# Performance work log

Measured on AMD Instinct MI355X. Metric: run time of the kernel, lower is better.

## Reference

```python
import jax, jax.numpy as jnp
import numpy as np

B, N_SRC, N_NGH = 2048, 1, 64
FEAT = EDGE = TIME = POS = 128
D_MODEL = FEAT + EDGE + TIME + POS  # 512
N_HEAD = 4
D_K = D_MODEL // N_HEAD  # 128
LN_EPS = 1e-5


def setup_inputs() -> dict:
    key = jax.random.key(0)
    ks = jax.random.split(key, 24)
    s = 0.05
    inp = {
        "src":   jax.random.normal(ks[0], (B, N_SRC, FEAT), jnp.float32),
        "src_t": jax.random.normal(ks[1], (B, N_SRC, TIME), jnp.float32),
        "src_p": jax.random.normal(ks[2], (B, N_SRC, POS), jnp.float32),
        "seq":   jax.random.normal(ks[3], (B, N_NGH, FEAT), jnp.float32),
        "seq_t": jax.random.normal(ks[4], (B, N_NGH, TIME), jnp.float32),
        "seq_e": jax.random.normal(ks[5], (B, N_NGH, EDGE), jnp.float32),
        "seq_p": jax.random.normal(ks[6], (B, N_NGH, POS), jnp.float32),
        "mask":  jax.random.randint(ks[7], (B, N_SRC, N_NGH), 0, 2).astype(bool),
        # MapBasedMultiHeadAttention params (Linear stored as [in, out])
        "Wq": jax.random.normal(ks[8],  (D_MODEL, N_HEAD * D_K), jnp.float32) * s,
        "Wk": jax.random.normal(ks[9],  (D_MODEL, N_HEAD * D_K), jnp.float32) * s,
        "Wv": jax.random.normal(ks[10], (D_MODEL, N_HEAD * D_K), jnp.float32) * s,
        "w_map": jax.random.normal(ks[11], (2 * D_K,), jnp.float32) * s,  # Linear(2*d_k, 1, bias=False)
        "fc_w": jax.random.normal(ks[12], (N_HEAD * D_K, D_MODEL), jnp.float32) * s,
        "fc_b": jnp.zeros((D_MODEL,), jnp.float32),
        "ln_g": jnp.ones((D_MODEL,), jnp.float32),
        "ln_b": jnp.zeros((D_MODEL,), jnp.float32),
        # MergeLayer(model_dim, feat_dim, feat_dim, feat_dim)
        "fc1_w": jax.random.normal(ks[13], (D_MODEL + FEAT, FEAT), jnp.float32) * s,
        "fc1_b": jnp.zeros((FEAT,), jnp.float32),
        "fc2_w": jax.random.normal(ks[14], (FEAT, FEAT), jnp.float32) * s,
        "fc2_b": jnp.zeros((FEAT,), jnp.float32),
    }
    return inp


def _forward(src, src_t, src_p, seq, seq_t, seq_e, seq_p, mask,
             Wq, Wk, Wv, w_map, fc_w, fc_b, ln_g, ln_b,
             fc1_w, fc1_b, fc2_w, fc2_b):
    b, ns, feat = src.shape
    nn = seq.shape[1]
    dk = w_map.shape[0] // 2
    h = Wq.shape[1] // dk

    # AttnModel: queries get zero edge features
    src_e = jnp.zeros((b, ns, seq_e.shape[-1]), src.dtype)
    q_in = jnp.concatenate([src, src_e, src_t, src_p], axis=-1)  # [B, Ns, D]
    k_in = jnp.concatenate([seq, seq_e, seq_t, seq_p], axis=-1)  # [B, Nn, D]

    qh = (q_in @ Wq).reshape(b, ns, h, dk)  # [B, Ns, H, dk]
    kh = (k_in @ Wk).reshape(b, nn, h, dk)  # [B, Nn, H, dk]
    vh = (k_in @ Wv).reshape(b, nn, h, dk)  # [B, Nn, H, dv]

    # weight_map(cat([q, k], -1)) == q . w_map[:dk] + k . w_map[dk:]
    # (linear in the concat -> decomposes into an outer sum; same math,
    #  avoids materializing the [H*B, Ns, Nn, 2*dk] concat tensor)
    q_score = jnp.einsum('bqhd,d->bhq', qh, w_map[:dk])
    k_score = jnp.einsum('bkhd,d->bhk', kh, w_map[dk:])
    attn = q_score[..., None] + k_score[:, :, None, :]  # [B, H, Ns, Nn]

    attn = jnp.where(mask[:, None, :, :], jnp.float32(-1e10), attn)
    attn = jax.nn.softmax(attn, axis=-1)

    out = jnp.einsum('bhqk,bkhd->bqhd', attn, vh).reshape(b, ns, h * dk)
    out = jax.nn.leaky_relu(out @ fc_w + fc_b, negative_slope=0.2)

    # residual + layernorm over d_model
    out = out + q_in
    mu = jnp.mean(out, axis=-1, keepdims=True)
    var = jnp.var(out, axis=-1, keepdims=True)
    out = (out - mu) * jax.lax.rsqrt(var + LN_EPS) * ln_g + ln_b

    # MergeLayer (non_linear=True)
    x = jnp.concatenate([out, src], axis=-1)  # [B, Ns, D+feat]
    z = jax.nn.relu(x @ fc1_w + fc1_b) @ fc2_w + fc2_b  # [B, Ns, feat]
    return z, attn


def reference(src, src_t, src_p, seq, seq_t, seq_e, seq_p, mask,
              Wq, Wk, Wv, w_map, fc_w, fc_b, ln_g, ln_b,
              fc1_w, fc1_b, fc2_w, fc2_b):
    return _forward(src, src_t, src_p, seq, seq_t, seq_e, seq_p, mask,
                    Wq, Wk, Wv, w_map, fc_w, fc_b, ln_g, ln_b,
                    fc1_w, fc1_b, fc2_w, fc2_b)
```

## Files before the change

### kernel.cpp

```cpp
#include <hip/hip_runtime.h>
#include <stdint.h>


#define DEV static __device__ __forceinline__

typedef __attribute__((ext_vector_type(8))) short short8;
typedef __attribute__((ext_vector_type(4))) float floatx4;

DEV unsigned short f2bf(float f) {
    unsigned int x; __builtin_memcpy(&x, &f, 4);
    return (unsigned short)((x + 0x7fffu + ((x >> 16) & 1u)) >> 16);
}
DEV unsigned int pk2(float hi, float lo) {
    unsigned int a, b;
    __builtin_memcpy(&a, &hi, 4); __builtin_memcpy(&b, &lo, 4);
    return __builtin_amdgcn_perm(a, b, 0x07060302u);
}

__global__ __launch_bounds__(256) void prep(const float* __restrict__ Wk,
                                            const float* __restrict__ w_map,
                                            const float* __restrict__ Wv,
                                            const float* __restrict__ fc_w,
                                            unsigned short* __restrict__ wkfrag,
                                            unsigned short* __restrict__ Gt) {
    const int t = threadIdx.x;
    if (blockIdx.x >= 256) {
        int n = (blockIdx.x - 256) * 256 + t;
        int h = n >> 9, c = n & 511;
        const float* wrow = Wk + (size_t)c * 512 + h * 128;
        const float* wm = w_map + 128;
        float acc = 0.f;
        #pragma unroll 8
        for (int d = 0; d < 128; d += 4) {
            float4 a = *(const float4*)(wrow + d);
            float4 b = *(const float4*)(wm + d);
            acc += a.x * b.x + a.y * b.y + a.z * b.z + a.w * b.w;
        }
        int kk = c >> 5, quad = (c >> 3) & 3, j = c & 7;
        unsigned short* p = wkfrag + (((kk * 4 + quad) * 16) + h) * 8 + j;
        p[0] = f2bf(acc);
        p[32] = 0; p[64] = 0; p[96] = 0;
        return;
    }
    __shared__ float wv[8 * 128];
    int r0 = blockIdx.x * 8;
    int h = r0 >> 9, c0 = r0 & 511;
    {
        int idx = t * 4;
        int i = idx >> 7, d = idx & 127;
        *(float4*)&wv[idx] = *(const float4*)(Wv + (size_t)(c0 + i) * 512 + h * 128 + d);
    }
    __syncthreads();
    float acc[8][2];
    #pragma unroll
    for (int i = 0; i < 8; i++) { acc[i][0] = 0.f; acc[i][1] = 0.f; }
    const float* fw = fc_w + (size_t)(h * 128) * 512 + t;
    for (int d = 0; d < 128; d++) {
        float w0 = fw[(size_t)d * 512];
        float w1 = fw[(size_t)d * 512 + 256];
        #pragma unroll
        for (int i = 0; i < 8; i++) {
            float a = wv[i * 128 + d];
            acc[i][0] += a * w0;
            acc[i][1] += a * w1;
        }
    }
    uint4 o0, o1;
    o0.x = ((unsigned int)f2bf(acc[1][0]) << 16) | f2bf(acc[0][0]);
    o0.y = ((unsigned int)f2bf(acc[3][0]) << 16) | f2bf(acc[2][0]);
    o0.z = ((unsigned int)f2bf(acc[5][0]) << 16) | f2bf(acc[4][0]);
    o0.w = ((unsigned int)f2bf(acc[7][0]) << 16) | f2bf(acc[6][0]);
    o1.x = ((unsigned int)f2bf(acc[1][1]) << 16) | f2bf(acc[0][1]);
    o1.y = ((unsigned int)f2bf(acc[3][1]) << 16) | f2bf(acc[2][1]);
    o1.z = ((unsigned int)f2bf(acc[5][1]) << 16) | f2bf(acc[4][1]);
    o1.w = ((unsigned int)f2bf(acc[7][1]) << 16) | f2bf(acc[6][1]);
    *(uint4*)(Gt + (size_t)t * 2048 + r0)         = o0;
    *(uint4*)(Gt + (size_t)(t + 256) * 2048 + r0) = o1;
}

__global__ __launch_bounds__(512, 4) void attn4(const float* __restrict__ seq,
                                                const float* __restrict__ seq_t,
                                                const float* __restrict__ seq_e,
                                                const float* __restrict__ seq_p,
                                                const int* __restrict__ mask,
                                                const unsigned short* __restrict__ wkfrag,
                                                float* __restrict__ attn_out,
                                                unsigned short* __restrict__ ctxb) {
    __shared__ __align__(16) unsigned short kinb[64 * 512];
    __shared__ float sd[64 * 5];
    __shared__ __align__(16) float pb[256];
    __shared__ __align__(16) float cb[4 * 512];
    const int b = blockIdx.x, t = threadIdx.x;
    const int w = t >> 6, l16 = t & 15, quad = (t >> 4) & 3;

    #pragma unroll
    for (int step = 0; step < 8; step++) {
        int g = step * 512 + t;
        int row = g >> 6, gcol = g & 63;
        int seg = gcol >> 4;
        const float* p = (seg == 0 ? seq : seg == 1 ? seq_e : seg == 2 ? seq_t : seq_p)
                         + (size_t)b * 8192 + row * 128 + (gcol & 15) * 8;
        float4 v0 = *(const float4*)p;
        float4 v1 = *(const float4*)(p + 4);
        uint4 pk;
        pk.x = pk2(v0.y, v0.x); pk.y = pk2(v0.w, v0.z);
        pk.z = pk2(v1.y, v1.x); pk.w = pk2(v1.w, v1.z);
        int ps = gcol ^ (row & 7) ^ ((row >> 3) & 7);
        *(uint4*)&kinb[row * 512 + ps * 8] = pk;
    }
    __syncthreads();

    if (w < 4) {
        short8 wkf[16];
        #pragma unroll
        for (int kk = 0; kk < 16; kk++)
            wkf[kk] = *(const short8*)(wkfrag + (((kk * 4 + quad) * 16) + l16) * 8);
        floatx4 sacc = {0.f, 0.f, 0.f, 0.f};
        const int srow = w * 16 + l16;
        const int rs = (srow & 7) ^ ((srow >> 3) & 7);
        #pragma unroll
        for (int kk = 0; kk < 16; kk++) {
            short8 af = *(const short8*)&kinb[srow * 512 + ((kk * 4 + quad) ^ rs) * 8];
            sacc = __builtin_amdgcn_mfma_f32_16x16x32_bf16(af, wkf[kk], sacc, 0, 0, 0);
        }
        if (l16 < 4) {
            #pragma unroll
            for (int r = 0; r < 4; r++) sd[(w * 16 + quad * 4 + r) * 5 + l16] = sacc[r];
        }
    }
    __syncthreads();

    if (t < 256) {
        int row = t & 63, head = t >> 6;
        float s = sd[row * 5 + head];
        float e = mask[b * 64 + row] ? 0.f : __expf(s);
        float sum = e;
        #pragma unroll
        for (int m = 32; m; m >>= 1) sum += __shfl_xor(sum, m, 64);
        float pr = e / sum;
        attn_out[b * 256 + t] = pr;
        pb[t] = pr;
    }
    __syncthreads();

    floatx4 cacc[4];
    #pragma unroll
    for (int nt = 0; nt < 4; nt++) cacc[nt] = (floatx4){0.f, 0.f, 0.f, 0.f};
    #pragma unroll
    for (int s = 0; s < 2; s++) {
        short8 afr = {0, 0, 0, 0, 0, 0, 0, 0};
        if (l16 < 4) {
            const float* pp = pb + l16 * 64 + s * 32 + quad * 8;
            float4 u0 = *(const float4*)pp;
            float4 u1 = *(const float4*)(pp + 4);
            uint4 tmp;
            tmp.x = pk2(u0.y, u0.x); tmp.y = pk2(u0.w, u0.z);
            tmp.z = pk2(u1.y, u1.x); tmp.w = pk2(u1.w, u1.z);
            __builtin_memcpy(&afr, &tmp, 16);
        }
        const int sq = s * 4 + quad;
        #pragma unroll
        for (int nt = 0; nt < 4; nt++) {
            const int c = w * 64 + nt * 16 + l16;
            const int gc = c >> 3, co = c & 7;
            short8 bfr;
            #pragma unroll
            for (int j = 0; j < 8; j++) {
                int r = s * 32 + quad * 8 + j;
                bfr[j] = (short)kinb[r * 512 + (gc ^ j ^ sq) * 8 + co];
            }
            cacc[nt] = __builtin_amdgcn_mfma_f32_16x16x32_bf16(afr, bfr, cacc[nt], 0, 0, 0);
        }
    }
    if (quad == 0) {
        #pragma unroll
        for (int nt = 0; nt < 4; nt++) {
            int c = w * 64 + nt * 16 + l16;
            #pragma unroll
            for (int r = 0; r < 4; r++) cb[r * 512 + c] = cacc[nt][r];
        }
    }
    __syncthreads();
    {
        const float* pp = cb + t * 4;
        float4 u = *(const float4*)pp;
        uint2 pk;
        pk.x = pk2(u.y, u.x); pk.y = pk2(u.w, u.z);
        *(uint2*)(ctxb + (size_t)b * 2048 + t * 4) = pk;
    }
}

__global__ __launch_bounds__(256) void gemm3(const unsigned short* __restrict__ A,
                                             const unsigned short* __restrict__ Bt,
                                             float* __restrict__ C) {
    __shared__ __align__(16) unsigned short As[32 * 64];
    __shared__ __align__(16) unsigned short Bs[64 * 64];
    const int t = threadIdx.x;
    const int m0 = blockIdx.x * 32, n0 = blockIdx.y * 64;
    const int w = t >> 6, lane = t & 63, quad = lane >> 4, l16 = lane & 15;
    const int wm = w >> 1, wn = w & 1;
    const int ar = t >> 3, g = t & 7;
    const int br0 = t >> 3, br1 = br0 + 32;
    const unsigned short* pa  = A  + (size_t)(m0 + ar) * 2048 + g * 8;
    const unsigned short* pb0 = Bt + (size_t)(n0 + br0) * 2048 + g * 8;
    const unsigned short* pb1 = Bt + (size_t)(n0 + br1) * 2048 + g * 8;
    const int da  = ar * 64 + (g ^ (ar & 7)) * 8;
    const int db0 = br0 * 64 + (g ^ (br0 & 7)) * 8;
    const int db1 = br1 * 64 + (g ^ (br1 & 7)) * 8;
    floatx4 acc0 = {0.f,0.f,0.f,0.f}, acc1 = {0.f,0.f,0.f,0.f};
    uint4 va = *(const uint4*)pa, vb0 = *(const uint4*)pb0, vb1 = *(const uint4*)pb1;
    const int ra = wm * 16 + l16, rb = wn * 32 + l16;
    for (int k0 = 0; k0 < 2048; k0 += 64) {
        *(uint4*)&As[da] = va; *(uint4*)&Bs[db0] = vb0; *(uint4*)&Bs[db1] = vb1;
        __syncthreads();
        if (k0 < 1984) {
            va  = *(const uint4*)(pa  + k0 + 64);
            vb0 = *(const uint4*)(pb0 + k0 + 64);
            vb1 = *(const uint4*)(pb1 + k0 + 64);
        }
        #pragma unroll
        for (int ks = 0; ks < 2; ks++) {
            int grp = ks * 4 + quad;
            short8 a  = *(const short8*)&As[ra * 64 + ((grp ^ (ra & 7)) * 8)];
            short8 b0 = *(const short8*)&Bs[rb * 64 + ((grp ^ (rb & 7)) * 8)];
            short8 b1 = *(const short8*)&Bs[(rb + 16) * 64 + ((grp ^ (rb & 7)) * 8)];
            acc0 = __builtin_amdgcn_mfma_f32_16x16x32_bf16(a, b0, acc0, 0, 0, 0);
            acc1 = __builtin_amdgcn_mfma_f32_16x16x32_bf16(a, b1, acc1, 0, 0, 0);
        }
        __syncthreads();
    }
    float* cp = C + (size_t)(m0 + wm * 16) * 512 + n0 + wn * 32;
    #pragma unroll
    for (int r = 0; r < 4; r++) {
        int rr = quad * 4 + r;
        cp[(size_t)rr * 512 + l16]      = acc0[r];
        cp[(size_t)rr * 512 + l16 + 16] = acc1[r];
    }
}

__global__ __launch_bounds__(256) void epilogue4(const float* __restrict__ out_pre,
                                                 const float* __restrict__ src,
                                                 const float* __restrict__ src_t,
                                                 const float* __restrict__ src_p,
                                                 const float* __restrict__ fc_b,
                                                 const float* __restrict__ ln_g,
                                                 const float* __restrict__ ln_b,
                                                 const float* __restrict__ fc1_w,
                                                 const float* __restrict__ fc1_b,
                                                 const float* __restrict__ fc2_w,
                                                 const float* __restrict__ fc2_b,
                                                 float* __restrict__ z_out) {
    __shared__ float oln[4][512];
    __shared__ float t1p[2][4][128];
    __shared__ float t1[4][128];
    const int t = threadIdx.x;
    const int b0 = blockIdx.x * 4;
    const int w = t >> 6, lane = t & 63;

    {
        int b = b0 + w;
        float vals[8];
        float sum = 0.f, ssq = 0.f;
        #pragma unroll
        for (int i = 0; i < 8; i++) {
            int c = lane + (i << 6);
            float v = out_pre[(size_t)b * 512 + c] + fc_b[c];
            v = (v > 0.f) ? v : 0.2f * v;
            float q;
            int seg = c >> 7;
            if (seg == 0)      q = src[b * 128 + c];
            else if (seg == 1) q = 0.f;
            else if (seg == 2) q = src_t[b * 128 + c - 256];
            else               q = src_p[b * 128 + c - 384];
            v += q;
            vals[i] = v;
            sum += v; ssq += v * v;
        }
        #pragma unroll
        for (int m = 32; m; m >>= 1) {
            sum += __shfl_xor(sum, m, 64);
            ssq += __shfl_xor(ssq, m, 64);
        }
        float mu = sum * (1.f / 512.f);
        float var = ssq * (1.f / 512.f) - mu * mu;
        float rstd = rsqrtf(var + 1e-5f);
        #pragma unroll
        for (int i = 0; i < 8; i++) {
            int c = lane + (i << 6);
            oln[w][c] = (vals[i] - mu) * rstd * ln_g[c] + ln_b[c];
        }
    }
    __syncthreads();

    {
        int j = t & 127, hf = t >> 7;
        float acc[4];
        #pragma unroll
        for (int bb = 0; bb < 4; bb++) acc[bb] = (hf == 0) ? fc1_b[j] : 0.f;
        int i0 = hf * 320;
        for (int ic = 0; ic < 320; ic += 4) {
            int i = i0 + ic;
            float w0 = fc1_w[(size_t)(i + 0) * 128 + j];
            float w1 = fc1_w[(size_t)(i + 1) * 128 + j];
            float w2 = fc1_w[(size_t)(i + 2) * 128 + j];
            float w3 = fc1_w[(size_t)(i + 3) * 128 + j];
            #pragma unroll
            for (int bb = 0; bb < 4; bb++) {
                float4 x;
                if (i < 512) x = *(const float4*)&oln[bb][i];
                else         x = *(const float4*)(src + (size_t)(b0 + bb) * 128 + (i - 512));
                acc[bb] += x.x * w0 + x.y * w1 + x.z * w2 + x.w * w3;
            }
        }
        #pragma unroll
        for (int bb = 0; bb < 4; bb++) t1p[hf][bb][j] = acc[bb];
    }
    __syncthreads();
    {
        int j = t & 127, g = t >> 7;
        #pragma unroll
        for (int e = 0; e < 2; e++) {
            int bb = g * 2 + e;
            t1[bb][j] = fmaxf(t1p[0][bb][j] + t1p[1][bb][j], 0.f);
        }
    }
    __syncthreads();
    {
        int j = t & 127, g = t >> 7;
        float acc[2];
        #pragma unroll
        for (int e = 0; e < 2; e++) acc[e] = fc2_b[j];
        for (int i = 0; i < 128; i++) {
            float w2 = fc2_w[(size_t)i * 128 + j];
            #pragma unroll
            for (int e = 0; e < 2; e++) acc[e] += t1[g * 2 + e][i] * w2;
        }
        #pragma unroll
        for (int e = 0; e < 2; e++)
            z_out[(size_t)(b0 + g * 2 + e) * 128 + j] = acc[e];
    }
}

extern "C" void kernel_launch(void* const* d_in, const int* in_sizes, int n_in,
                              void* d_out, int out_size, void* d_ws, size_t ws_size,
                              hipStream_t stream) {
    const float* src   = (const float*)d_in[0];
    const float* src_t = (const float*)d_in[1];
    const float* src_p = (const float*)d_in[2];
    const float* seq   = (const float*)d_in[3];
    const float* seq_t = (const float*)d_in[4];
    const float* seq_e = (const float*)d_in[5];
    const float* seq_p = (const float*)d_in[6];
    const int*   mask  = (const int*)d_in[7];
    const float* Wk    = (const float*)d_in[9];
    const float* Wv    = (const float*)d_in[10];
    const float* w_map = (const float*)d_in[11];
    const float* fc_w  = (const float*)d_in[12];
    const float* fc_b  = (const float*)d_in[13];
    const float* ln_g  = (const float*)d_in[14];
    const float* ln_b  = (const float*)d_in[15];
    const float* fc1_w = (const float*)d_in[16];
    const float* fc1_b = (const float*)d_in[17];
    const float* fc2_w = (const float*)d_in[18];
    const float* fc2_b = (const float*)d_in[19];

    float* z_out    = (float*)d_out;
    float* attn_out = (float*)d_out + 2048 * 128;

    char* ws = (char*)d_ws;
    unsigned short* wkfrag  = (unsigned short*)ws;
    unsigned short* Gt      = (unsigned short*)(ws + 65536);
    unsigned short* ctxb    = (unsigned short*)(ws + 65536 + (2u << 20));
    float*          out_pre = (float*)(ws + 65536 + (10u << 20));

    hipLaunchKernelGGL(prep, dim3(264), dim3(256), 0, stream,
                       Wk, w_map, Wv, fc_w, wkfrag, Gt);
    hipLaunchKernelGGL(attn4, dim3(2048), dim3(512), 0, stream,
                       seq, seq_t, seq_e, seq_p, mask, wkfrag, attn_out, ctxb);
    hipLaunchKernelGGL(gemm3, dim3(64, 8), dim3(256), 0, stream, ctxb, Gt, out_pre);
    hipLaunchKernelGGL(epilogue4, dim3(512), dim3(256), 0, stream, out_pre,
                       src, src_t, src_p, fc_b, ln_g, ln_b,
                       fc1_w, fc1_b, fc2_w, fc2_b, z_out);
}
```

Measured before the change: 368.6 us.

## Make attention blocks loop over eight batches with double-buffered LDS prefetch

The attention kernel now runs 256 blocks, and each block handles eight consecutive batch rows instead of one. The global loads for the next batch's neighbor features are issued into registers before the current batch's score and context MFMAs run, then converted and written into a second LDS buffer, so load latency overlaps compute. The Wk fragment registers are loaded once per block instead of once per batch. In exchange, LDS use doubles to two 64KB buffers and each thread holds 64 more registers, which lowers resident blocks per CU. Fewer, longer blocks may also leave latency exposed if one block per CU cannot keep memory busy.

```diff
diff --git a/kernel.cpp b/kernel.cpp
--- a/kernel.cpp
+++ b/kernel.cpp
@@ -78,7 +78,7 @@
     *(uint4*)(Gt + (size_t)(t + 256) * 2048 + r0) = o1;
 }
 
-__global__ __launch_bounds__(512, 4) void attn4(const float* __restrict__ seq,
+__global__ __launch_bounds__(512, 2) void attn5(const float* __restrict__ seq,
                                                 const float* __restrict__ seq_t,
                                                 const float* __restrict__ seq_e,
                                                 const float* __restrict__ seq_p,
@@ -86,12 +86,20 @@
                                                 const unsigned short* __restrict__ wkfrag,
                                                 float* __restrict__ attn_out,
                                                 unsigned short* __restrict__ ctxb) {
-    __shared__ __align__(16) unsigned short kinb[64 * 512];
+    __shared__ __align__(16) unsigned short kin[2][64 * 512];
     __shared__ float sd[64 * 5];
     __shared__ __align__(16) float pb[256];
     __shared__ __align__(16) float cb[4 * 512];
-    const int b = blockIdx.x, t = threadIdx.x;
+    const int t = threadIdx.x;
     const int w = t >> 6, l16 = t & 15, quad = (t >> 4) & 3;
+    const int b0 = blockIdx.x * 8;
+
+    short8 wkf[16];
+    if (w < 4) {
+        #pragma unroll
+        for (int kk = 0; kk < 16; kk++)
+            wkf[kk] = *(const short8*)(wkfrag + (((kk * 4 + quad) * 16) + l16) * 8);
+    }
 
     #pragma unroll
     for (int step = 0; step < 8; step++) {
@@ -99,94 +107,125 @@
         int row = g >> 6, gcol = g & 63;
         int seg = gcol >> 4;
         const float* p = (seg == 0 ? seq : seg == 1 ? seq_e : seg == 2 ? seq_t : seq_p)
-                         + (size_t)b * 8192 + row * 128 + (gcol & 15) * 8;
+                         + (size_t)b0 * 8192 + row * 128 + (gcol & 15) * 8;
         float4 v0 = *(const float4*)p;
         float4 v1 = *(const float4*)(p + 4);
         uint4 pk;
         pk.x = pk2(v0.y, v0.x); pk.y = pk2(v0.w, v0.z);
         pk.z = pk2(v1.y, v1.x); pk.w = pk2(v1.w, v1.z);
         int ps = gcol ^ (row & 7) ^ ((row >> 3) & 7);
-        *(uint4*)&kinb[row * 512 + ps * 8] = pk;
+        *(uint4*)&kin[0][row * 512 + ps * 8] = pk;
     }
     __syncthreads();
 
-    if (w < 4) {
-        short8 wkf[16];
-        #pragma unroll
-        for (int kk = 0; kk < 16; kk++)
-            wkf[kk] = *(const short8*)(wkfrag + (((kk * 4 + quad) * 16) + l16) * 8);
-        floatx4 sacc = {0.f, 0.f, 0.f, 0.f};
-        const int srow = w * 16 + l16;
-        const int rs = (srow & 7) ^ ((srow >> 3) & 7);
-        #pragma unroll
-        for (int kk = 0; kk < 16; kk++) {
-            short8 af = *(const short8*)&kinb[srow * 512 + ((kk * 4 + quad) ^ rs) * 8];
-            sacc = __builtin_amdgcn_mfma_f32_16x16x32_bf16(af, wkf[kk], sacc, 0, 0, 0);
-        }
-        if (l16 < 4) {
-            #pragma unroll
-            for (int r = 0; r < 4; r++) sd[(w * 16 + quad * 4 + r) * 5 + l16] = sacc[r];
-        }
-    }
-    __syncthreads();
-
-    if (t < 256) {
-        int row = t & 63, head = t >> 6;
-        float s = sd[row * 5 + head];
-        float e = mask[b * 64 + row] ? 0.f : __expf(s);
-        float sum = e;
-        #pragma unroll
-        for (int m = 32; m; m >>= 1) sum += __shfl_xor(sum, m, 64);
-        float pr = e / sum;
-        attn_out[b * 256 + t] = pr;
-        pb[t] = pr;
-    }
-    __syncthreads();
-
-    floatx4 cacc[4];
-    #pragma unroll
-    for (int nt = 0; nt < 4; nt++) cacc[nt] = (floatx4){0.f, 0.f, 0.f, 0.f};
-    #pragma unroll
-    for (int s = 0; s < 2; s++) {
-        short8 afr = {0, 0, 0, 0, 0, 0, 0, 0};
-        if (l16 < 4) {
-            const float* pp = pb + l16 * 64 + s * 32 + quad * 8;
-            float4 u0 = *(const float4*)pp;
-            float4 u1 = *(const float4*)(pp + 4);
-            uint4 tmp;
-            tmp.x = pk2(u0.y, u0.x); tmp.y = pk2(u0.w, u0.z);
-            tmp.z = pk2(u1.y, u1.x); tmp.w = pk2(u1.w, u1.z);
-            __builtin_memcpy(&afr, &tmp, 16);
-        }
-        const int sq = s * 4 + quad;
-        #pragma unroll
-        for (int nt = 0; nt < 4; nt++) {
-            const int c = w * 64 + nt * 16 + l16;
-            const int gc = c >> 3, co = c & 7;
-            short8 bfr;
-            #pragma unroll
-            for (int j = 0; j < 8; j++) {
-                int r = s * 32 + quad * 8 + j;
-                bfr[j] = (short)kinb[r * 512 + (gc ^ j ^ sq) * 8 + co];
-            }
-            cacc[nt] = __builtin_amdgcn_mfma_f32_16x16x32_bf16(afr, bfr, cacc[nt], 0, 0, 0);
-        }
-    }
-    if (quad == 0) {
-        #pragma unroll
-        for (int nt = 0; nt < 4; nt++) {
-            int c = w * 64 + nt * 16 + l16;
-            #pragma unroll
-            for (int r = 0; r < 4; r++) cb[r * 512 + c] = cacc[nt][r];
-        }
-    }
-    __syncthreads();
-    {
-        const float* pp = cb + t * 4;
-        float4 u = *(const float4*)pp;
-        uint2 pk;
-        pk.x = pk2(u.y, u.x); pk.y = pk2(u.w, u.z);
-        *(uint2*)(ctxb + (size_t)b * 2048 + t * 4) = pk;
+    for (int i = 0; i < 8; i++) {
+        const int cur = i & 1;
+        const int bi = b0 + i;
+
+        float4 sv0[8], sv1[8];
+        if (i < 7) {
+            #pragma unroll
+            for (int step = 0; step < 8; step++) {
+                int g = step * 512 + t;
+                int row = g >> 6, gcol = g & 63;
+                int seg = gcol >> 4;
+                const float* p = (seg == 0 ? seq : seg == 1 ? seq_e : seg == 2 ? seq_t : seq_p)
+                                 + (size_t)(bi + 1) * 8192 + row * 128 + (gcol & 15) * 8;
+                sv0[step] = *(const float4*)p;
+                sv1[step] = *(const float4*)(p + 4);
+            }
+        }
+        int mk = 0;
+        if (t < 256) mk = mask[bi * 64 + (t & 63)];
+
+        if (w < 4) {
+            floatx4 sacc = {0.f, 0.f, 0.f, 0.f};
+            const int srow = w * 16 + l16;
+            const int rs = (srow & 7) ^ ((srow >> 3) & 7);
+            #pragma unroll
+            for (int kk = 0; kk < 16; kk++) {
+                short8 af = *(const short8*)&kin[cur][srow * 512 + ((kk * 4 + quad) ^ rs) * 8];
+                sacc = __builtin_amdgcn_mfma_f32_16x16x32_bf16(af, wkf[kk], sacc, 0, 0, 0);
+            }
+            if (l16 < 4) {
+                #pragma unroll
+                for (int r = 0; r < 4; r++) sd[(w * 16 + quad * 4 + r) * 5 + l16] = sacc[r];
+            }
+        }
+        __syncthreads();
+
+        if (t < 256) {
+            int row = t & 63;
+            float s = sd[row * 5 + (t >> 6)];
+            float e = mk ? 0.f : __expf(s);
+            float sum = e;
+            #pragma unroll
+            for (int m = 32; m; m >>= 1) sum += __shfl_xor(sum, m, 64);
+            float pr = e / sum;
+            attn_out[bi * 256 + t] = pr;
+            pb[t] = pr;
+        }
+        __syncthreads();
+
+        floatx4 cacc[4];
+        #pragma unroll
+        for (int nt = 0; nt < 4; nt++) cacc[nt] = (floatx4){0.f, 0.f, 0.f, 0.f};
+        #pragma unroll
+        for (int s = 0; s < 2; s++) {
+            short8 afr = {0, 0, 0, 0, 0, 0, 0, 0};
+            if (l16 < 4) {
+                const float* pp = pb + l16 * 64 + s * 32 + quad * 8;
+                float4 u0 = *(const float4*)pp;
+                float4 u1 = *(const float4*)(pp + 4);
+                uint4 tmp;
+                tmp.x = pk2(u0.y, u0.x); tmp.y = pk2(u0.w, u0.z);
+                tmp.z = pk2(u1.y, u1.x); tmp.w = pk2(u1.w, u1.z);
+                __builtin_memcpy(&afr, &tmp, 16);
+            }
+            const int sq = s * 4 + quad;
+            #pragma unroll
+            for (int nt = 0; nt < 4; nt++) {
+                const int c = w * 64 + nt * 16 + l16;
+                const int gc = c >> 3, co = c & 7;
+                short8 bfr;
+                #pragma unroll
+                for (int j = 0; j < 8; j++) {
+                    int r = s * 32 + quad * 8 + j;
+                    bfr[j] = (short)kin[cur][r * 512 + (gc ^ j ^ sq) * 8 + co];
+                }
+                cacc[nt] = __builtin_amdgcn_mfma_f32_16x16x32_bf16(afr, bfr, cacc[nt], 0, 0, 0);
+            }
+        }
+        if (quad == 0) {
+            #pragma unroll
+            for (int nt = 0; nt < 4; nt++) {
+                int c = w * 64 + nt * 16 + l16;
+                #pragma unroll
+                for (int r = 0; r < 4; r++) cb[r * 512 + c] = cacc[nt][r];
+            }
+        }
+
+        if (i < 7) {
+            #pragma unroll
+            for (int step = 0; step < 8; step++) {
+                int g = step * 512 + t;
+                int row = g >> 6, gcol = g & 63;
+                uint4 pk;
+                pk.x = pk2(sv0[step].y, sv0[step].x); pk.y = pk2(sv0[step].w, sv0[step].z);
+                pk.z = pk2(sv1[step].y, sv1[step].x); pk.w = pk2(sv1[step].w, sv1[step].z);
+                int ps = gcol ^ (row & 7) ^ ((row >> 3) & 7);
+                *(uint4*)&kin[cur ^ 1][row * 512 + ps * 8] = pk;
+            }
+        }
+        __syncthreads();
+
+        {
+            const float* pp = cb + t * 4;
+            float4 u = *(const float4*)pp;
+            uint2 pk;
+            pk.x = pk2(u.y, u.x); pk.y = pk2(u.w, u.z);
+            *(uint2*)(ctxb + (size_t)bi * 2048 + t * 4) = pk;
+        }
     }
 }
 
@@ -375,7 +414,7 @@
 
     hipLaunchKernelGGL(prep, dim3(264), dim3(256), 0, stream,
                        Wk, w_map, Wv, fc_w, wkfrag, Gt);
-    hipLaunchKernelGGL(attn4, dim3(2048), dim3(512), 0, stream,
+    hipLaunchKernelGGL(attn5, dim3(256), dim3(512), 0, stream,
                        seq, seq_t, seq_e, seq_p, mask, wkfrag, attn_out, ctxb);
     hipLaunchKernelGGL(gemm3, dim3(64, 8), dim3(256), 0, stream, ctxb, Gt, out_pre);
     hipLaunchKernelGGL(epilogue4, dim3(512), dim3(256), 0, stream, out_pre,
```

Measured after the change: 381.4 us. 3.5% more time.
